# Optimization experiments

Hardware: AMD Instinct MI355X
Metric: run time of the kernel (lower is better)

## Reference

```python
import jax, jax.numpy as jnp
import numpy as np

EPS = 1e-5
NEG_SLOPE = 0.01  # F.leaky_relu default

N0, N1, N2 = 100000, 25000, 5000
E0, E1 = 800000, 160000
D_IN, D_HID, D_OUT = 256, 256, 128


def setup_inputs() -> dict:
    key = jax.random.key(0)
    ks = jax.random.split(key, 16)
    inp = {
        "x": jax.random.normal(ks[0], (N0, D_IN), dtype=jnp.float32),
        "src0": jax.random.randint(ks[1], (E0,), 0, N0, dtype=jnp.int32),
        "dst0": jax.random.randint(ks[2], (E0,), 0, N1, dtype=jnp.int32),
        "val0": jnp.arange(E0, dtype=jnp.int32),
        "src1": jax.random.randint(ks[3], (E1,), 0, N1, dtype=jnp.int32),
        "dst1": jax.random.randint(ks[4], (E1,), 0, N2, dtype=jnp.int32),
        "val1": jnp.arange(E1, dtype=jnp.int32),
        "timestamps": jax.random.randint(ks[5], (E0 + E1,), 0, 100, dtype=jnp.int32),
        "time": 50,
        "interval": 10,
        # SAGEConv layer 1 (in -> hidden): lin_l (bias) on aggregated, lin_r (no bias) on root
        "W1l": jax.random.normal(ks[6], (D_IN, D_HID), dtype=jnp.float32) / np.sqrt(D_IN),
        "W1r": jax.random.normal(ks[7], (D_IN, D_HID), dtype=jnp.float32) / np.sqrt(D_IN),
        "b1": jnp.zeros((D_HID,), dtype=jnp.float32),
        # BatchNorm1d params (eval mode: running stats)
        "g1": jnp.ones((D_HID,), dtype=jnp.float32),
        "bt1": jnp.zeros((D_HID,), dtype=jnp.float32),
        "rm1": jax.random.normal(ks[8], (D_HID,), dtype=jnp.float32) * 0.1,
        "rv1": jax.random.uniform(ks[9], (D_HID,), dtype=jnp.float32) + 0.5,
        # SAGEConv layer 2 (hidden -> out)
        "W2l": jax.random.normal(ks[10], (D_HID, D_OUT), dtype=jnp.float32) / np.sqrt(D_HID),
        "W2r": jax.random.normal(ks[11], (D_HID, D_OUT), dtype=jnp.float32) / np.sqrt(D_HID),
        "b2": jnp.zeros((D_OUT,), dtype=jnp.float32),
    }
    return inp


def _time_mask(val, timestamps, time, interval):
    # time_sparse keeps edges whose timestamp is in {time, ..., time+interval-1}
    ts = timestamps[val]
    return (ts >= time) & (ts < time + interval)


def _sage_conv(x_src, x_tgt, src, dst, mask, Wl, Wr, b, n_tgt):
    m = mask.astype(x_src.dtype)
    msg = x_src[src] * m[:, None]               # [E, D] gather + mask
    agg = jax.ops.segment_sum(msg, dst, num_segments=n_tgt)
    deg = jax.ops.segment_sum(m, dst, num_segments=n_tgt)
    agg = agg / jnp.maximum(deg, 1.0)[:, None]  # mean aggregation
    return agg @ Wl + b + x_tgt @ Wr


def reference(x, src0, dst0, val0, src1, dst1, val1, timestamps, time, interval,
              W1l, W1r, b1, g1, bt1, rm1, rv1, W2l, W2r, b2):
    # layer 0: N0 -> N1
    mask0 = _time_mask(val0, timestamps, time, interval)
    h = _sage_conv(x, x[:N1], src0, dst0, mask0, W1l, W1r, b1, N1)
    # BatchNorm1d (eval) + leaky_relu; dropout is identity in eval
    h = (h - rm1) * jax.lax.rsqrt(rv1 + EPS) * g1 + bt1
    h = jnp.where(h >= 0, h, NEG_SLOPE * h)
    # layer 1: N1 -> N2
    mask1 = _time_mask(val1, timestamps, time, interval)
    out = _sage_conv(h, h[:N2], src1, dst1, mask1, W2l, W2r, b2, N2)
    return out, mask1
```

## Files before the change

kernel.cpp:

```cpp
#include <hip/hip_runtime.h>

#define N1c 25000
#define N2c 5000
#define Dc 256
#define DOUTc 128
#define EPSc 1e-5f
#define NEGc 0.01f

typedef __attribute__((ext_vector_type(8))) short short8;
typedef __attribute__((ext_vector_type(4))) float f32x4;

__device__ __forceinline__ ushort f2bf(float f) {
    unsigned u = __float_as_uint(f);
    u += 0x7fffu + ((u >> 16) & 1u);
    return (ushort)(u >> 16);
}
__device__ __forceinline__ float bf2f(ushort u) {
    return __uint_as_float(((unsigned)u) << 16);
}
__device__ __forceinline__ unsigned pack2(float lo, float hi) {
    return ((unsigned)f2bf(lo)) | (((unsigned)f2bf(hi)) << 16);
}

__global__ __launch_bounds__(256) void prep_all(
    const int* __restrict__ dst0, const int* __restrict__ val0,
    const int* __restrict__ dst1, const int* __restrict__ val1,
    const int* __restrict__ ts, const int* __restrict__ time_p, const int* __restrict__ itv_p,
    const float* __restrict__ W1l, const float* __restrict__ W1r,
    const float* __restrict__ W2l, const float* __restrict__ W2r,
    int E0, int E1,
    ushort* __restrict__ Bt1, ushort* __restrict__ Bt2,
    int* __restrict__ count0, int* __restrict__ count1) {
    const int flat = blockIdx.x * blockDim.x + threadIdx.x;
    const int NT = gridDim.x * blockDim.x;
    const int t0 = *time_p, iv = *itv_p;

    for (int i = flat; i < 256 * 512; i += NT) {
        int n = i >> 9, k = i & 511;
        float v = (k < 256) ? W1l[(size_t)k * 256 + n] : W1r[(size_t)(k - 256) * 256 + n];
        Bt1[i] = f2bf(v);
    }
    for (int i = flat; i < 128 * 512; i += NT) {
        int n = i >> 9, k = i & 511;
        float v = (k < 256) ? W2l[(size_t)k * 128 + n] : W2r[(size_t)(k - 256) * 128 + n];
        Bt2[i] = f2bf(v);
    }
    for (int e = flat; e < E0; e += NT) {
        int t = ts[val0[e]];
        if (t >= t0 && t < t0 + iv) atomicAdd(&count0[dst0[e]], 1);
    }
    for (int e = flat; e < E1; e += NT) {
        int t = ts[val1[e]];
        if (t >= t0 && t < t0 + iv) atomicAdd(&count1[dst1[e]], 1);
    }
}

template <int CH>
__device__ __forceinline__ void scan_block(const int* __restrict__ count,
                                           int* __restrict__ offsets, int n) {
    __shared__ int wsum[16];
    int t = threadIdx.x;
    int lane = t & 63, w = t >> 6;
    int v[CH];
    int base = t * CH;
    int run = 0;
#pragma unroll
    for (int i = 0; i < CH; ++i) {
        int c = (base + i < n) ? count[base + i] : 0;
        v[i] = run;
        run += c;
    }
    int incl = run;
#pragma unroll
    for (int off = 1; off < 64; off <<= 1) {
        int s = __shfl_up(incl, off, 64);
        if (lane >= off) incl += s;
    }
    if (lane == 63) wsum[w] = incl;
    __syncthreads();
    if (t == 0) {
        int s = 0;
#pragma unroll
        for (int i = 0; i < 16; ++i) { int c = wsum[i]; wsum[i] = s; s += c; }
    }
    __syncthreads();
    int pre = wsum[w] + (incl - run);
#pragma unroll
    for (int i = 0; i < CH; ++i) {
        int idx = base + i;
        if (idx < n) offsets[idx] = pre + v[i];
    }
}

__global__ __launch_bounds__(1024) void scan_both(
    const int* __restrict__ count0, int* __restrict__ offsets0,
    const int* __restrict__ count1, int* __restrict__ offsets1) {
    if (blockIdx.x == 0) scan_block<25>(count0, offsets0, N1c);
    else                 scan_block<5>(count1, offsets1, N2c);
}

__global__ __launch_bounds__(256) void fill_both(
    const int* __restrict__ src0, const int* __restrict__ dst0, const int* __restrict__ val0,
    const int* __restrict__ src1, const int* __restrict__ dst1, const int* __restrict__ val1,
    const int* __restrict__ ts, const int* __restrict__ time_p, const int* __restrict__ itv_p,
    int E0, int E1,
    int* __restrict__ offsets0, int* __restrict__ offsets1,
    int* __restrict__ eidx0, int* __restrict__ eidx1,
    float* __restrict__ mask_out) {
    int e = blockIdx.x * blockDim.x + threadIdx.x;
    int t0 = *time_p, iv = *itv_p;
    if (e < E0) {
        int t = ts[val0[e]];
        if (t >= t0 && t < t0 + iv) {
            int pos = atomicAdd(&offsets0[dst0[e]], 1);
            eidx0[pos] = src0[e];
        }
    } else if (e < E0 + E1) {
        int e1 = e - E0;
        int t = ts[val1[e1]];
        bool m = (t >= t0 && t < t0 + iv);
        mask_out[e1] = m ? 1.0f : 0.0f;
        if (m) {
            int pos = atomicAdd(&offsets1[dst1[e1]], 1);
            eidx1[pos] = src1[e1];
        }
    }
}

__global__ void gather_f32(const float* __restrict__ X,
                           const int* __restrict__ off,
                           const int* __restrict__ eidx,
                           ushort* __restrict__ agg, int n) {
    int wave = (blockIdx.x * blockDim.x + threadIdx.x) >> 6;
    int lane = threadIdx.x & 63;
    if (wave >= n) return;
    int s1 = off[wave];
    int s0 = wave ? off[wave - 1] : 0;
    float4 acc = make_float4(0.f, 0.f, 0.f, 0.f);
    for (int j = s0; j < s1; ++j) {
        int s = eidx[j];
        float4 v = *(const float4*)(X + (size_t)s * Dc + lane * 4);
        acc.x += v.x; acc.y += v.y; acc.z += v.z; acc.w += v.w;
    }
    float inv = 1.0f / fmaxf((float)(s1 - s0), 1.0f);
    ushort4 o;
    o.x = f2bf(acc.x * inv); o.y = f2bf(acc.y * inv);
    o.z = f2bf(acc.z * inv); o.w = f2bf(acc.w * inv);
    *(ushort4*)(agg + (size_t)wave * Dc + lane * 4) = o;
}

__global__ void gather_bf16(const ushort* __restrict__ H,
                            const int* __restrict__ off,
                            const int* __restrict__ eidx,
                            ushort* __restrict__ agg, int n) {
    int wave = (blockIdx.x * blockDim.x + threadIdx.x) >> 6;
    int lane = threadIdx.x & 63;
    if (wave >= n) return;
    int s1 = off[wave];
    int s0 = wave ? off[wave - 1] : 0;
    float4 acc = make_float4(0.f, 0.f, 0.f, 0.f);
    for (int j = s0; j < s1; ++j) {
        int s = eidx[j];
        ushort4 v = *(const ushort4*)(H + (size_t)s * Dc + lane * 4);
        acc.x += bf2f(v.x); acc.y += bf2f(v.y);
        acc.z += bf2f(v.z); acc.w += bf2f(v.w);
    }
    float inv = 1.0f / fmaxf((float)(s1 - s0), 1.0f);
    ushort4 o;
    o.x = f2bf(acc.x * inv); o.y = f2bf(acc.y * inv);
    o.z = f2bf(acc.z * inv); o.w = f2bf(acc.w * inv);
    *(ushort4*)(agg + (size_t)wave * Dc + lane * 4) = o;
}

template <int VARIANT, int GRPS>
__global__ __launch_bounds__(128) void gemm_mfma(
    const ushort* __restrict__ Alo,
    const ushort* __restrict__ A2b, const float* __restrict__ A2f,
    const ushort* __restrict__ Bt,
    const float* __restrict__ bias,
    const float* __restrict__ g, const float* __restrict__ bt,
    const float* __restrict__ rm, const float* __restrict__ rv,
    void* __restrict__ Cout, int M) {
    constexpr int BM = 32 * GRPS;
    constexpr int TPR = 128 / BM;
    constexpr int CHUNK = 32 / TPR;
    __shared__ ushort As[BM][40];
    __shared__ ushort Bs[128][40];
    int tid = threadIdx.x;
    int wave = tid >> 6, lane = tid & 63;
    int quad = lane >> 4, l16 = lane & 15;
    int m0 = blockIdx.y * BM, n0 = blockIdx.x * 128;
    f32x4 acc[GRPS][8] = {};
    int ar = tid / TPR;
    int ak = (tid % TPR) * CHUNK;
    int bn = tid;
    for (int k0 = 0; k0 < 512; k0 += 32) {
        uint4 a0 = make_uint4(0, 0, 0, 0), a1 = make_uint4(0, 0, 0, 0);
        bool inb = (m0 + ar) < M;
        if (k0 < 256) {
            if (inb) {
                const ushort* Ag = Alo + (size_t)(m0 + ar) * Dc + k0 + ak;
                a0 = *(const uint4*)Ag;
                if (CHUNK == 16) a1 = *(const uint4*)(Ag + 8);
            }
        } else if (VARIANT == 0) {
            if (inb) {
                const float* Af = A2f + (size_t)(m0 + ar) * Dc + (k0 - 256) + ak;
                float4 f0 = *(const float4*)(Af + 0);
                float4 f1 = *(const float4*)(Af + 4);
                a0 = make_uint4(pack2(f0.x, f0.y), pack2(f0.z, f0.w),
                                pack2(f1.x, f1.y), pack2(f1.z, f1.w));
                if (CHUNK == 16) {
                    float4 f2 = *(const float4*)(Af + 8);
                    float4 f3 = *(const float4*)(Af + 12);
                    a1 = make_uint4(pack2(f2.x, f2.y), pack2(f2.z, f2.w),
                                    pack2(f3.x, f3.y), pack2(f3.z, f3.w));
                }
            }
        } else {
            if (inb) {
                const ushort* Ag = A2b + (size_t)(m0 + ar) * Dc + (k0 - 256) + ak;
                a0 = *(const uint4*)Ag;
                if (CHUNK == 16) a1 = *(const uint4*)(Ag + 8);
            }
        }
        const ushort* Bg = Bt + (size_t)(n0 + bn) * 512 + k0;
        uint4 b0 = *(const uint4*)(Bg + 0);
        uint4 b1 = *(const uint4*)(Bg + 8);
        uint4 b2 = *(const uint4*)(Bg + 16);
        uint4 b3 = *(const uint4*)(Bg + 24);
        __syncthreads();
        *(uint4*)&As[ar][ak] = a0;
        if (CHUNK == 16) *(uint4*)&As[ar][ak + 8] = a1;
        *(uint4*)&Bs[bn][0] = b0;
        *(uint4*)&Bs[bn][8] = b1;
        *(uint4*)&Bs[bn][16] = b2;
        *(uint4*)&Bs[bn][24] = b3;
        __syncthreads();
        short8 af[GRPS];
#pragma unroll
        for (int grp = 0; grp < GRPS; ++grp)
            af[grp] = *(const short8*)&As[wave * 16 * GRPS + grp * 16 + l16][quad * 8];
#pragma unroll
        for (int j = 0; j < 8; ++j) {
            short8 bf = *(const short8*)&Bs[j * 16 + l16][quad * 8];
#pragma unroll
            for (int grp = 0; grp < GRPS; ++grp)
                acc[grp][j] = __builtin_amdgcn_mfma_f32_16x16x32_bf16(af[grp], bf, acc[grp][j], 0, 0, 0);
        }
    }
#pragma unroll
    for (int grp = 0; grp < GRPS; ++grp) {
#pragma unroll
        for (int j = 0; j < 8; ++j) {
            int gn = n0 + j * 16 + l16;
            float sc = 1.f, sh = bias[gn];
            if (VARIANT == 0) {
                float s = g[gn] * rsqrtf(rv[gn] + EPSc);
                sh = (bias[gn] - rm[gn]) * s + bt[gn];
                sc = s;
            }
            int gmb = m0 + wave * 16 * GRPS + grp * 16 + quad * 4;
#pragma unroll
            for (int r = 0; r < 4; ++r) {
                int gm = gmb + r;
                if (gm >= M) continue;
                float v = acc[grp][j][r];
                if (VARIANT == 0) {
                    v = v * sc + sh;
                    v = v >= 0.f ? v : NEGc * v;
                    ((ushort*)Cout)[(size_t)gm * Dc + gn] = f2bf(v);
                } else {
                    ((float*)Cout)[(size_t)gm * DOUTc + gn] = v + sh;
                }
            }
        }
    }
}

extern "C" void kernel_launch(void* const* d_in, const int* in_sizes, int n_in,
                              void* d_out, int out_size, void* d_ws, size_t ws_size,
                              hipStream_t stream) {
    const float* x    = (const float*)d_in[0];
    const int* src0   = (const int*)d_in[1];
    const int* dst0   = (const int*)d_in[2];
    const int* val0   = (const int*)d_in[3];
    const int* src1   = (const int*)d_in[4];
    const int* dst1   = (const int*)d_in[5];
    const int* val1   = (const int*)d_in[6];
    const int* ts     = (const int*)d_in[7];
    const int* time_p = (const int*)d_in[8];
    const int* itv_p  = (const int*)d_in[9];
    const float* W1l  = (const float*)d_in[10];
    const float* W1r  = (const float*)d_in[11];
    const float* b1   = (const float*)d_in[12];
    const float* g1   = (const float*)d_in[13];
    const float* bt1  = (const float*)d_in[14];
    const float* rm1  = (const float*)d_in[15];
    const float* rv1  = (const float*)d_in[16];
    const float* W2l  = (const float*)d_in[17];
    const float* W2r  = (const float*)d_in[18];
    const float* b2   = (const float*)d_in[19];
    int E0 = in_sizes[1];
    int E1 = in_sizes[4];
    float* out = (float*)d_out;

    ushort* agg0 = (ushort*)d_ws;
    ushort* h    = agg0 + (size_t)N1c * Dc;
    ushort* agg1 = h    + (size_t)N1c * Dc;
    ushort* Bt1  = agg1 + (size_t)N2c * Dc;
    ushort* Bt2  = Bt1  + 256 * 512;
    int* ip      = (int*)(Bt2 + 128 * 512);
    int* count0   = ip;            ip += N1c;
    int* count1   = ip;            ip += N2c;
    int* offsets0 = ip;            ip += N1c;
    int* offsets1 = ip;            ip += N2c;
    int* eidx0    = ip;            ip += E0;
    int* eidx1    = ip;            ip += E1;
    float* mask_tail = out + (size_t)N2c * DOUTc;

    hipMemsetAsync(count0, 0, (size_t)(N1c + N2c) * sizeof(int), stream);

    prep_all<<<1024, 256, 0, stream>>>(
        dst0, val0, dst1, val1, ts, time_p, itv_p,
        W1l, W1r, W2l, W2r, E0, E1, Bt1, Bt2, count0, count1);
    scan_both<<<2, 1024, 0, stream>>>(count0, offsets0, count1, offsets1);
    fill_both<<<(E0 + E1 + 255) / 256, 256, 0, stream>>>(
        src0, dst0, val0, src1, dst1, val1, ts, time_p, itv_p,
        E0, E1, offsets0, offsets1, eidx0, eidx1, mask_tail);
    gather_f32<<<(N1c + 3) / 4, 256, 0, stream>>>(x, offsets0, eidx0, agg0, N1c);
    gemm_mfma<0, 2><<<dim3(2, (N1c + 63) / 64), 128, 0, stream>>>(
        agg0, nullptr, x, Bt1, b1, g1, bt1, rm1, rv1, h, N1c);
    gather_bf16<<<(N2c + 3) / 4, 256, 0, stream>>>(h, offsets1, eidx1, agg1, N2c);
    gemm_mfma<1, 1><<<dim3(1, (N2c + 31) / 32), 128, 0, stream>>>(
        agg1, h, nullptr, Bt2, b2, nullptr, nullptr, nullptr, nullptr, out, N2c);
}
```

Before: 279.9 us.

## Replace CSR scan/fill with fixed-capacity per-destination buckets and fallback

Removes the prefix-scan and separate fill kernels by writing masked edge sources directly into fixed 32-slot buckets per destination during the counting pass. The gather kernels load bucket indices into lanes and broadcast them with shuffles, unrolled by two with dual accumulators. Destinations that overflow the cap fall back to a full linear scan over all edges. This saves two launches and a serial single-block scan, at the cost of a larger index buffer and a slow fallback path for high-degree nodes.

```diff
diff --git a/kernel.cpp b/kernel.cpp
--- a/kernel.cpp
+++ b/kernel.cpp
@@ -6,6 +6,7 @@
 #define DOUTc 128
 #define EPSc 1e-5f
 #define NEGc 0.01f
+#define CAPc 32
 
 typedef __attribute__((ext_vector_type(8))) short short8;
 typedef __attribute__((ext_vector_type(4))) float f32x4;
@@ -22,15 +23,17 @@
     return ((unsigned)f2bf(lo)) | (((unsigned)f2bf(hi)) << 16);
 }
 
-__global__ __launch_bounds__(256) void prep_all(
-    const int* __restrict__ dst0, const int* __restrict__ val0,
-    const int* __restrict__ dst1, const int* __restrict__ val1,
+__global__ __launch_bounds__(256) void prep_fill(
+    const int* __restrict__ src0, const int* __restrict__ dst0, const int* __restrict__ val0,
+    const int* __restrict__ src1, const int* __restrict__ dst1, const int* __restrict__ val1,
     const int* __restrict__ ts, const int* __restrict__ time_p, const int* __restrict__ itv_p,
     const float* __restrict__ W1l, const float* __restrict__ W1r,
     const float* __restrict__ W2l, const float* __restrict__ W2r,
     int E0, int E1,
     ushort* __restrict__ Bt1, ushort* __restrict__ Bt2,
-    int* __restrict__ count0, int* __restrict__ count1) {
+    int* __restrict__ cnt0, int* __restrict__ cnt1,
+    int* __restrict__ eidx0, int* __restrict__ eidx1,
+    float* __restrict__ mask_out) {
     const int flat = blockIdx.x * blockDim.x + threadIdx.x;
     const int NT = gridDim.x * blockDim.x;
     const int t0 = *time_p, iv = *itv_p;
@@ -47,102 +50,67 @@
     }
     for (int e = flat; e < E0; e += NT) {
         int t = ts[val0[e]];
-        if (t >= t0 && t < t0 + iv) atomicAdd(&count0[dst0[e]], 1);
+        if (t >= t0 && t < t0 + iv) {
+            int d = dst0[e];
+            int pos = atomicAdd(&cnt0[d], 1);
+            if (pos < CAPc) eidx0[d * CAPc + pos] = src0[e];
+        }
     }
     for (int e = flat; e < E1; e += NT) {
         int t = ts[val1[e]];
-        if (t >= t0 && t < t0 + iv) atomicAdd(&count1[dst1[e]], 1);
-    }
-}
-
-template <int CH>
-__device__ __forceinline__ void scan_block(const int* __restrict__ count,
-                                           int* __restrict__ offsets, int n) {
-    __shared__ int wsum[16];
-    int t = threadIdx.x;
-    int lane = t & 63, w = t >> 6;
-    int v[CH];
-    int base = t * CH;
-    int run = 0;
-#pragma unroll
-    for (int i = 0; i < CH; ++i) {
-        int c = (base + i < n) ? count[base + i] : 0;
-        v[i] = run;
-        run += c;
-    }
-    int incl = run;
-#pragma unroll
-    for (int off = 1; off < 64; off <<= 1) {
-        int s = __shfl_up(incl, off, 64);
-        if (lane >= off) incl += s;
-    }
-    if (lane == 63) wsum[w] = incl;
-    __syncthreads();
-    if (t == 0) {
-        int s = 0;
-#pragma unroll
-        for (int i = 0; i < 16; ++i) { int c = wsum[i]; wsum[i] = s; s += c; }
-    }
-    __syncthreads();
-    int pre = wsum[w] + (incl - run);
-#pragma unroll
-    for (int i = 0; i < CH; ++i) {
-        int idx = base + i;
-        if (idx < n) offsets[idx] = pre + v[i];
-    }
-}
-
-__global__ __launch_bounds__(1024) void scan_both(
-    const int* __restrict__ count0, int* __restrict__ offsets0,
-    const int* __restrict__ count1, int* __restrict__ offsets1) {
-    if (blockIdx.x == 0) scan_block<25>(count0, offsets0, N1c);
-    else                 scan_block<5>(count1, offsets1, N2c);
-}
-
-__global__ __launch_bounds__(256) void fill_both(
-    const int* __restrict__ src0, const int* __restrict__ dst0, const int* __restrict__ val0,
-    const int* __restrict__ src1, const int* __restrict__ dst1, const int* __restrict__ val1,
-    const int* __restrict__ ts, const int* __restrict__ time_p, const int* __restrict__ itv_p,
-    int E0, int E1,
-    int* __restrict__ offsets0, int* __restrict__ offsets1,
-    int* __restrict__ eidx0, int* __restrict__ eidx1,
-    float* __restrict__ mask_out) {
-    int e = blockIdx.x * blockDim.x + threadIdx.x;
-    int t0 = *time_p, iv = *itv_p;
-    if (e < E0) {
-        int t = ts[val0[e]];
-        if (t >= t0 && t < t0 + iv) {
-            int pos = atomicAdd(&offsets0[dst0[e]], 1);
-            eidx0[pos] = src0[e];
-        }
-    } else if (e < E0 + E1) {
-        int e1 = e - E0;
-        int t = ts[val1[e1]];
         bool m = (t >= t0 && t < t0 + iv);
-        mask_out[e1] = m ? 1.0f : 0.0f;
+        mask_out[e] = m ? 1.0f : 0.0f;
         if (m) {
-            int pos = atomicAdd(&offsets1[dst1[e1]], 1);
-            eidx1[pos] = src1[e1];
+            int d = dst1[e];
+            int pos = atomicAdd(&cnt1[d], 1);
+            if (pos < CAPc) eidx1[d * CAPc + pos] = src1[e];
         }
     }
 }
 
 __global__ void gather_f32(const float* __restrict__ X,
-                           const int* __restrict__ off,
+                           const int* __restrict__ cnt,
                            const int* __restrict__ eidx,
+                           const int* __restrict__ src, const int* __restrict__ dst,
+                           const int* __restrict__ val, const int* __restrict__ ts,
+                           const int* __restrict__ time_p, const int* __restrict__ itv_p,
+                           int E,
                            ushort* __restrict__ agg, int n) {
     int wave = (blockIdx.x * blockDim.x + threadIdx.x) >> 6;
     int lane = threadIdx.x & 63;
     if (wave >= n) return;
-    int s1 = off[wave];
-    int s0 = wave ? off[wave - 1] : 0;
+    int c = cnt[wave];
     float4 acc = make_float4(0.f, 0.f, 0.f, 0.f);
-    for (int j = s0; j < s1; ++j) {
-        int s = eidx[j];
-        float4 v = *(const float4*)(X + (size_t)s * Dc + lane * 4);
-        acc.x += v.x; acc.y += v.y; acc.z += v.z; acc.w += v.w;
-    }
-    float inv = 1.0f / fmaxf((float)(s1 - s0), 1.0f);
+    float4 acc2 = make_float4(0.f, 0.f, 0.f, 0.f);
+    if (c <= CAPc) {
+        int my = (lane < c) ? eidx[wave * CAPc + lane] : 0;
+        int j = 0;
+        for (; j + 1 < c; j += 2) {
+            int s0 = __shfl(my, j, 64);
+            int s1 = __shfl(my, j + 1, 64);
+            float4 v0 = *(const float4*)(X + (size_t)s0 * Dc + lane * 4);
+            float4 v1 = *(const float4*)(X + (size_t)s1 * Dc + lane * 4);
+            acc.x += v0.x; acc.y += v0.y; acc.z += v0.z; acc.w += v0.w;
+            acc2.x += v1.x; acc2.y += v1.y; acc2.z += v1.z; acc2.w += v1.w;
+        }
+        if (j < c) {
+            int s0 = __shfl(my, j, 64);
+            float4 v0 = *(const float4*)(X + (size_t)s0 * Dc + lane * 4);
+            acc.x += v0.x; acc.y += v0.y; acc.z += v0.z; acc.w += v0.w;
+        }
+    } else {
+        int t0 = *time_p, iv = *itv_p;
+        for (int e = 0; e < E; ++e) {
+            if (dst[e] != wave) continue;
+            int t = ts[val[e]];
+            if (t >= t0 && t < t0 + iv) {
+                float4 v = *(const float4*)(X + (size_t)src[e] * Dc + lane * 4);
+                acc.x += v.x; acc.y += v.y; acc.z += v.z; acc.w += v.w;
+            }
+        }
+    }
+    acc.x += acc2.x; acc.y += acc2.y; acc.z += acc2.z; acc.w += acc2.w;
+    float inv = 1.0f / fmaxf((float)c, 1.0f);
     ushort4 o;
     o.x = f2bf(acc.x * inv); o.y = f2bf(acc.y * inv);
     o.z = f2bf(acc.z * inv); o.w = f2bf(acc.w * inv);
@@ -150,22 +118,52 @@
 }
 
 __global__ void gather_bf16(const ushort* __restrict__ H,
-                            const int* __restrict__ off,
+                            const int* __restrict__ cnt,
                             const int* __restrict__ eidx,
+                            const int* __restrict__ src, const int* __restrict__ dst,
+                            const int* __restrict__ val, const int* __restrict__ ts,
+                            const int* __restrict__ time_p, const int* __restrict__ itv_p,
+                            int E,
                             ushort* __restrict__ agg, int n) {
     int wave = (blockIdx.x * blockDim.x + threadIdx.x) >> 6;
     int lane = threadIdx.x & 63;
     if (wave >= n) return;
-    int s1 = off[wave];
-    int s0 = wave ? off[wave - 1] : 0;
+    int c = cnt[wave];
     float4 acc = make_float4(0.f, 0.f, 0.f, 0.f);
-    for (int j = s0; j < s1; ++j) {
-        int s = eidx[j];
-        ushort4 v = *(const ushort4*)(H + (size_t)s * Dc + lane * 4);
-        acc.x += bf2f(v.x); acc.y += bf2f(v.y);
-        acc.z += bf2f(v.z); acc.w += bf2f(v.w);
-    }
-    float inv = 1.0f / fmaxf((float)(s1 - s0), 1.0f);
+    float4 acc2 = make_float4(0.f, 0.f, 0.f, 0.f);
+    if (c <= CAPc) {
+        int my = (lane < c) ? eidx[wave * CAPc + lane] : 0;
+        int j = 0;
+        for (; j + 1 < c; j += 2) {
+            int s0 = __shfl(my, j, 64);
+            int s1 = __shfl(my, j + 1, 64);
+            ushort4 v0 = *(const ushort4*)(H + (size_t)s0 * Dc + lane * 4);
+            ushort4 v1 = *(const ushort4*)(H + (size_t)s1 * Dc + lane * 4);
+            acc.x += bf2f(v0.x); acc.y += bf2f(v0.y);
+            acc.z += bf2f(v0.z); acc.w += bf2f(v0.w);
+            acc2.x += bf2f(v1.x); acc2.y += bf2f(v1.y);
+            acc2.z += bf2f(v1.z); acc2.w += bf2f(v1.w);
+        }
+        if (j < c) {
+            int s0 = __shfl(my, j, 64);
+            ushort4 v0 = *(const ushort4*)(H + (size_t)s0 * Dc + lane * 4);
+            acc.x += bf2f(v0.x); acc.y += bf2f(v0.y);
+            acc.z += bf2f(v0.z); acc.w += bf2f(v0.w);
+        }
+    } else {
+        int t0 = *time_p, iv = *itv_p;
+        for (int e = 0; e < E; ++e) {
+            if (dst[e] != wave) continue;
+            int t = ts[val[e]];
+            if (t >= t0 && t < t0 + iv) {
+                ushort4 v = *(const ushort4*)(H + (size_t)src[e] * Dc + lane * 4);
+                acc.x += bf2f(v.x); acc.y += bf2f(v.y);
+                acc.z += bf2f(v.z); acc.w += bf2f(v.w);
+            }
+        }
+    }
+    acc.x += acc2.x; acc.y += acc2.y; acc.z += acc2.z; acc.w += acc2.w;
+    float inv = 1.0f / fmaxf((float)c, 1.0f);
     ushort4 o;
     o.x = f2bf(acc.x * inv); o.y = f2bf(acc.y * inv);
     o.z = f2bf(acc.z * inv); o.w = f2bf(acc.w * inv);
@@ -311,27 +309,24 @@
     ushort* Bt1  = agg1 + (size_t)N2c * Dc;
     ushort* Bt2  = Bt1  + 256 * 512;
     int* ip      = (int*)(Bt2 + 128 * 512);
-    int* count0   = ip;            ip += N1c;
-    int* count1   = ip;            ip += N2c;
-    int* offsets0 = ip;            ip += N1c;
-    int* offsets1 = ip;            ip += N2c;
-    int* eidx0    = ip;            ip += E0;
-    int* eidx1    = ip;            ip += E1;
+    int* cnt0    = ip;             ip += N1c;
+    int* cnt1    = ip;             ip += N2c;
+    int* eidx0   = ip;             ip += N1c * CAPc;
+    int* eidx1   = ip;             ip += N2c * CAPc;
     float* mask_tail = out + (size_t)N2c * DOUTc;
 
-    hipMemsetAsync(count0, 0, (size_t)(N1c + N2c) * sizeof(int), stream);
-
-    prep_all<<<1024, 256, 0, stream>>>(
-        dst0, val0, dst1, val1, ts, time_p, itv_p,
-        W1l, W1r, W2l, W2r, E0, E1, Bt1, Bt2, count0, count1);
-    scan_both<<<2, 1024, 0, stream>>>(count0, offsets0, count1, offsets1);
-    fill_both<<<(E0 + E1 + 255) / 256, 256, 0, stream>>>(
+    hipMemsetAsync(cnt0, 0, (size_t)(N1c + N2c) * sizeof(int), stream);
+
+    prep_fill<<<2048, 256, 0, stream>>>(
         src0, dst0, val0, src1, dst1, val1, ts, time_p, itv_p,
-        E0, E1, offsets0, offsets1, eidx0, eidx1, mask_tail);
-    gather_f32<<<(N1c + 3) / 4, 256, 0, stream>>>(x, offsets0, eidx0, agg0, N1c);
+        W1l, W1r, W2l, W2r, E0, E1, Bt1, Bt2,
+        cnt0, cnt1, eidx0, eidx1, mask_tail);
+    gather_f32<<<(N1c + 3) / 4, 256, 0, stream>>>(
+        x, cnt0, eidx0, src0, dst0, val0, ts, time_p, itv_p, E0, agg0, N1c);
     gemm_mfma<0, 2><<<dim3(2, (N1c + 63) / 64), 128, 0, stream>>>(
         agg0, nullptr, x, Bt1, b1, g1, bt1, rm1, rv1, h, N1c);
-    gather_bf16<<<(N2c + 3) / 4, 256, 0, stream>>>(h, offsets1, eidx1, agg1, N2c);
+    gather_bf16<<<(N2c + 3) / 4, 256, 0, stream>>>(
+        h, cnt1, eidx1, src1, dst1, val1, ts, time_p, itv_p, E1, agg1, N2c);
     gemm_mfma<1, 1><<<dim3(1, (N2c + 31) / 32), 128, 0, stream>>>(
         agg1, h, nullptr, Bt2, b2, nullptr, nullptr, nullptr, nullptr, out, N2c);
 }
```

Result: faster. 254.2 us (-9.2%).
